# Kernel optimization log

Hardware: AMD Instinct MI355X
Metric: run time of the kernel (lower is better)

## Reference

```python
import jax, jax.numpy as jnp
import numpy as np

B, S, C, H, D = 2, 2048, 1024, 16, 64  # hidden C must equal H*D (value is a reshape of key_states)


def setup_inputs() -> dict:
    key = jax.random.key(0)
    ks = jax.random.split(key, 7)
    query_states = jax.random.normal(ks[0], (B, S, C), dtype=jnp.float32)
    key_states = jax.random.normal(ks[1], (B, S, C), dtype=jnp.float32)
    attention_mask = jax.random.randint(ks[2], (B, 1, 1, S), 0, 2).astype(jnp.int32)
    Wq = jax.random.normal(ks[3], (C, H, D), dtype=jnp.float32) * 0.02
    bq = jnp.zeros((H, D), dtype=jnp.float32)
    Wk = jax.random.normal(ks[4], (C, H, D), dtype=jnp.float32) * 0.02
    bk = jnp.zeros((H, D), dtype=jnp.float32)
    return {
        "query_states": query_states,
        "key_states": key_states,
        "attention_mask": attention_mask,
        "Wq": Wq,
        "bq": bq,
        "Wk": Wk,
        "bk": bk,
    }


def reference(query_states, key_states, attention_mask, Wq, bq, Wk, bk):
    # EinsumDense 'abc,cde->abde' with bias on 'de'
    q = jnp.einsum("bsc,chd->bshd", query_states, Wq) + bq  # [B,S,H,D]
    k = jnp.einsum("bsc,chd->bshd", key_states, Wk) + bk    # [B,S,H,D]
    # value is just key_states reshaped into head layout (no projection!)
    v = key_states.reshape(k.shape)                          # [B,S,H,D]
    # scale query by 1/sqrt(dk)
    q = q * jax.lax.rsqrt(jnp.asarray(D, q.dtype))
    # 'aecd,abcd->acbe': a=batch, c=head, b=query pos, e=key pos
    scores = jnp.einsum("bkhd,bqhd->bhqk", k, q)             # [B,H,Sq,Sk]
    mask = (1.0 - attention_mask.astype(scores.dtype)) * -10000.0
    scores = scores + mask
    probs = jax.nn.softmax(scores, axis=-1)
    # dropout is identity at training=False (default)
    # 'acbe,aecd->abcd': weighted sum of values over key positions
    out = jnp.einsum("bhqk,bkhd->bqhd", probs, v)            # [B,S,H,D]
    return out
```

## Files before the change

### kernel.cpp

```cpp
#include <hip/hip_runtime.h>

#define BSZ 2
#define SEQ 2048
#define CH  1024
#define NH  16
#define HD  64
#define LOG2E 1.4426950408889634f
#define MASKC (-14426.950408889634f)

typedef short  bf16x8 __attribute__((ext_vector_type(8)));
typedef short  bf16x4 __attribute__((ext_vector_type(4)));
typedef float  f32x4  __attribute__((ext_vector_type(4)));

__device__ __forceinline__ short f2bf(float f) {
    union { float f; unsigned u; } v; v.f = f;
    unsigned r = v.u + 0x7FFFu + ((v.u >> 16) & 1u);
    return (short)(r >> 16);
}
__device__ __forceinline__ short f2bf_fast(float f) {
    union { float f; unsigned u; } v; v.f = f;
    return (short)((v.u + 0x8000u) >> 16);
}
__device__ __forceinline__ float exp2_hw(float x) {
#if __has_builtin(__builtin_amdgcn_exp2f)
    return __builtin_amdgcn_exp2f(x);
#else
    float r;
    asm volatile("v_exp_f32 %0, %1\n\ts_nop 1" : "=v"(r) : "v"(x));
    return r;
#endif
}

#if __has_builtin(__builtin_amdgcn_mfma_f32_16x16x16bf16_1k)
__device__ __forceinline__ f32x4 mfma16x16x16(bf16x4 a, bf16x4 b, f32x4 c) {
    return __builtin_amdgcn_mfma_f32_16x16x16bf16_1k(a, b, c, 0, 0, 0);
}
#else
__device__ __forceinline__ f32x4 mfma16x16x16(bf16x4 a, bf16x4 b, f32x4 c) {
    f32x4 d;
    asm("v_mfma_f32_16x16x16_bf16 %0, %1, %2, %3"
        : "=v"(d) : "v"(a), "v"(b), "v"(c));
    return d;
}
#endif

__global__ __launch_bounds__(256) void prep(
    const float* __restrict__ query, const float* __restrict__ key,
    const float* __restrict__ Wq, const float* __restrict__ Wk,
    short* __restrict__ qc, short* __restrict__ kc,
    short* __restrict__ wtq, short* __restrict__ wtk,
    short* __restrict__ vtr)
{
    __shared__ float tile[64][65];
    const int bid = blockIdx.x;
    const int tid = threadIdx.x;

    if (bid < 4096) {
        const float* s = (bid < 2048) ? query : key;
        short*       d = (bid < 2048) ? qc : kc;
        long i = ((long)(bid & 2047) * 256 + tid) * 8;
        float4 v0 = *(const float4*)&s[i];
        float4 v1 = *(const float4*)&s[i + 4];
        bf16x8 o;
        o[0] = f2bf(v0.x); o[1] = f2bf(v0.y); o[2] = f2bf(v0.z); o[3] = f2bf(v0.w);
        o[4] = f2bf(v1.x); o[5] = f2bf(v1.y); o[6] = f2bf(v1.z); o[7] = f2bf(v1.w);
        *(bf16x8*)&d[i] = o;
        return;
    }

    const float* s; short* d;
    int r0, c0, srs, drs;
    if (bid < 4608) {
        int t = bid - 4096;
        s   = (t < 256) ? Wq : Wk;
        d   = (t < 256) ? wtq : wtk;
        t  &= 255;
        r0  = (t >> 4) * 64;
        c0  = (t & 15) * 64;
        srs = CH; drs = CH;
    } else {
        int t = bid - 4608;
        int z = t >> 5;
        int sy = t & 31;
        s   = key + (long)(z >> 4) * SEQ * CH + (long)(z & 15) * HD;
        d   = vtr + (long)z * HD * SEQ;
        r0  = sy * 64;
        c0  = 0;
        srs = CH; drs = SEQ;
    }

    const int r  = tid >> 2;
    const int c4 = (tid & 3) << 4;
    #pragma unroll
    for (int i = 0; i < 16; i += 4) {
        float4 v = *(const float4*)&s[(long)(r0 + r) * srs + c0 + c4 + i];
        tile[r][c4 + i + 0] = v.x;
        tile[r][c4 + i + 1] = v.y;
        tile[r][c4 + i + 2] = v.z;
        tile[r][c4 + i + 3] = v.w;
    }
    __syncthreads();
    bf16x8 o0, o1;
    #pragma unroll
    for (int i = 0; i < 8; i++) o0[i] = f2bf(tile[c4 + i][r]);
    #pragma unroll
    for (int i = 0; i < 8; i++) o1[i] = f2bf(tile[c4 + 8 + i][r]);
    *(bf16x8*)&d[(long)(c0 + r) * drs + r0 + c4 + 0] = o0;
    *(bf16x8*)&d[(long)(c0 + r) * drs + r0 + c4 + 8] = o1;
}

__global__ __launch_bounds__(256, 2) void proj_mfma(
    const short* __restrict__ Xq, const short* __restrict__ Xk,
    const short* __restrict__ Wtq, const short* __restrict__ Wtk,
    const float* __restrict__ bq_, const float* __restrict__ bk_,
    short* __restrict__ Yq, short* __restrict__ Yk)
{
    __shared__ short At[2][128 * 72];
    __shared__ short Bt[2][128 * 72];

    const int bid  = blockIdx.x;
    const int g    = bid >> 3, xcd = bid & 7;
    const int pair = ((g >> 3) << 3) | xcd;
    const int xt   = g & 7;
    const int yy   = pair >> 1;
    const int zz   = pair & 1;

    const short* X    = zz ? Xk  : Xq;
    const short* Wt   = zz ? Wtk : Wtq;
    const float* bias = zz ? bk_ : bq_;
    short*       Y    = zz ? Yk  : Yq;
    const float scale = zz ? 1.0f : (0.125f * LOG2E);

    const int tid  = threadIdx.x;
    const int lane = tid & 63, w = tid >> 6;
    const int quad = lane >> 4, t16 = lane & 15;
    const int m0 = yy * 128, n0 = xt * 128;
    const int srow = tid >> 1;
    const int shalf = (tid & 1) * 32;

    f32x4 acc[4][4];
    #pragma unroll
    for (int i = 0; i < 4; i++)
        #pragma unroll
        for (int j = 0; j < 4; j++)
            acc[i][j] = (f32x4){0.f, 0.f, 0.f, 0.f};

    const int M0 = (w >> 1) * 64, N0 = (w & 1) * 64;
    const int NIT = CH / 64;

    bf16x8 ar[4], br[4];
    #pragma unroll
    for (int c = 0; c < 4; c++) {
        ar[c] = *(const bf16x8*)&X [(long)(m0 + srow) * CH + shalf + 8 * c];
        br[c] = *(const bf16x8*)&Wt[(long)(n0 + srow) * CH + shalf + 8 * c];
    }
    #pragma unroll
    for (int c = 0; c < 4; c++) {
        *(bf16x8*)&At[0][srow * 72 + shalf + 8 * c] = ar[c];
        *(bf16x8*)&Bt[0][srow * 72 + shalf + 8 * c] = br[c];
    }
    #pragma unroll
    for (int c = 0; c < 4; c++) {
        ar[c] = *(const bf16x8*)&X [(long)(m0 + srow) * CH + 64 + shalf + 8 * c];
        br[c] = *(const bf16x8*)&Wt[(long)(n0 + srow) * CH + 64 + shalf + 8 * c];
    }
    __syncthreads();

    for (int it = 0; it < NIT; it++) {
        const int buf = it & 1;
        if (it + 1 < NIT) {
            #pragma unroll
            for (int c = 0; c < 4; c++) {
                *(bf16x8*)&At[buf ^ 1][srow * 72 + shalf + 8 * c] = ar[c];
                *(bf16x8*)&Bt[buf ^ 1][srow * 72 + shalf + 8 * c] = br[c];
            }
            if (it + 2 < NIT) {
                const long ko = (long)(it + 2) * 64;
                #pragma unroll
                for (int c = 0; c < 4; c++) {
                    ar[c] = *(const bf16x8*)&X [(long)(m0 + srow) * CH + ko + shalf + 8 * c];
                    br[c] = *(const bf16x8*)&Wt[(long)(n0 + srow) * CH + ko + shalf + 8 * c];
                }
            }
        }

        #pragma unroll
        for (int kk = 0; kk < 2; kk++) {
            bf16x8 af[4], bw[4];
            #pragma unroll
            for (int im = 0; im < 4; im++)
                af[im] = *(bf16x8*)&At[buf][(M0 + 16 * im + t16) * 72 + kk * 32 + quad * 8];
            #pragma unroll
            for (int jn = 0; jn < 4; jn++)
                bw[jn] = *(bf16x8*)&Bt[buf][(N0 + 16 * jn + t16) * 72 + kk * 32 + quad * 8];
            #pragma unroll
            for (int im = 0; im < 4; im++)
                #pragma unroll
                for (int jn = 0; jn < 4; jn++)
                    acc[im][jn] = __builtin_amdgcn_mfma_f32_16x16x32_bf16(
                        af[im], bw[jn], acc[im][jn], 0, 0, 0);
        }
        __syncthreads();
    }

    #pragma unroll
    for (int jn = 0; jn < 4; jn++) {
        float bs = bias[n0 + N0 + 16 * jn + t16];
        #pragma unroll
        for (int im = 0; im < 4; im++)
            #pragma unroll
            for (int reg = 0; reg < 4; reg++) {
                float y = (acc[im][jn][reg] + bs) * scale;
                Y[(long)(m0 + M0 + 16 * im + 4 * quad + reg) * (NH * HD)
                  + n0 + N0 + 16 * jn + t16] = f2bf(y);
            }
    }
}

__global__ __launch_bounds__(256, 2) void attn_mfma(
    const short* __restrict__ qp,
    const short* __restrict__ kp,
    const short* __restrict__ vt,
    const int*   __restrict__ amask,
    float* __restrict__ out)
{
    __shared__ short Kt[2][128 * 72];
    __shared__ short Vt[2][64 * 136];
    __shared__ float Msk[SEQ];

    const int bid = blockIdx.x;
    const int g   = bid >> 3, xcd = bid & 7;
    const int hb  = ((g >> 4) << 3) | xcd;
    const int qt  = g & 15;

    const int qt0 = qt * 128;
    const int h   = hb & 15;
    const int b   = hb >> 4;
    const int tid = threadIdx.x;
    const int lane = tid & 63, w = tid >> 6;
    const int quad = lane >> 4, t16 = lane & 15;

    {
        int4 a0 = *(const int4*)&amask[b * SEQ + tid * 8];
        int4 a1 = *(const int4*)&amask[b * SEQ + tid * 8 + 4];
        float4 f0 = {a0.x ? 0.f : MASKC, a0.y ? 0.f : MASKC,
                     a0.z ? 0.f : MASKC, a0.w ? 0.f : MASKC};
        float4 f1 = {a1.x ? 0.f : MASKC, a1.y ? 0.f : MASKC,
                     a1.z ? 0.f : MASKC, a1.w ? 0.f : MASKC};
        *(float4*)&Msk[tid * 8]     = f0;
        *(float4*)&Msk[tid * 8 + 4] = f1;
    }

    bf16x8 qf[2][2];
    #pragma unroll
    for (int qm = 0; qm < 2; qm++)
        #pragma unroll
        for (int ds = 0; ds < 2; ds++)
            qf[qm][ds] = *(const bf16x8*)&qp[
                (long)(b * SEQ + qt0 + w * 32 + qm * 16 + t16) * CH
                + h * HD + ds * 32 + quad * 8];

    f32x4 oa[4][2];
    float l_r[2];
    #pragma unroll
    for (int dt = 0; dt < 4; dt++)
        #pragma unroll
        for (int qm = 0; qm < 2; qm++)
            oa[dt][qm] = (f32x4){0.f, 0.f, 0.f, 0.f};
    l_r[0] = l_r[1] = 0.f;

    const int ksrow = tid >> 1;
    const int kscol = (tid & 1) * 32;
    const int vsrow = tid >> 2;
    const int vscol = (tid & 3) * 32;
    const long kbase = (long)(b * SEQ) * CH + h * HD;
    const long vbase = ((long)(b * NH + h) * HD) * SEQ;
    const int NIT = SEQ / 128;

    bf16x8 kr[4], vr[4];
    #pragma unroll
    for (int c = 0; c < 4; c++) {
        kr[c] = *(const bf16x8*)&kp[kbase + (long)ksrow * CH + kscol + 8 * c];
        vr[c] = *(const bf16x8*)&vt[vbase + (long)vsrow * SEQ + vscol + 8 * c];
    }
    #pragma unroll
    for (int c = 0; c < 4; c++) {
        *(bf16x8*)&Kt[0][ksrow * 72 + kscol + 8 * c] = kr[c];
        *(bf16x8*)&Vt[0][vsrow * 136 + vscol + 8 * c] = vr[c];
    }
    #pragma unroll
    for (int c = 0; c < 4; c++) {
        kr[c] = *(const bf16x8*)&kp[kbase + (long)(128 + ksrow) * CH + kscol + 8 * c];
        vr[c] = *(const bf16x8*)&vt[vbase + (long)vsrow * SEQ + 128 + vscol + 8 * c];
    }
    __syncthreads();

    for (int it = 0; it < NIT; it++) {
        const int buf = it & 1;
        const int kt0 = it * 128;

        if (it + 1 < NIT) {
            #pragma unroll
            for (int c = 0; c < 4; c++) {
                *(bf16x8*)&Kt[buf ^ 1][ksrow * 72 + kscol + 8 * c] = kr[c];
                *(bf16x8*)&Vt[buf ^ 1][vsrow * 136 + vscol + 8 * c] = vr[c];
            }
            if (it + 2 < NIT) {
                const int kn = kt0 + 256;
                #pragma unroll
                for (int c = 0; c < 4; c++) {
                    kr[c] = *(const bf16x8*)&kp[kbase + (long)(kn + ksrow) * CH + kscol + 8 * c];
                    vr[c] = *(const bf16x8*)&vt[vbase + (long)vsrow * SEQ + kn + vscol + 8 * c];
                }
            }
        }

        #pragma unroll
        for (int sub = 0; sub < 2; sub++) {
            const int ko = sub * 64;

            float4 mv4[4];
            #pragma unroll
            for (int jt = 0; jt < 4; jt++)
                mv4[jt] = *(const float4*)&Msk[kt0 + ko + jt * 16 + quad * 4];

            f32x4 sa[2][4];
            #pragma unroll
            for (int qm = 0; qm < 2; qm++)
                #pragma unroll
                for (int jt = 0; jt < 4; jt++)
                    sa[qm][jt] = (f32x4){mv4[jt].x, mv4[jt].y, mv4[jt].z, mv4[jt].w};
            #pragma unroll
            for (int ds = 0; ds < 2; ds++) {
                bf16x8 kb[4];
                #pragma unroll
                for (int jt = 0; jt < 4; jt++)
                    kb[jt] = *(bf16x8*)&Kt[buf][(ko + jt * 16 + t16) * 72 + ds * 32 + quad * 8];
                __builtin_amdgcn_s_setprio(1);
                #pragma unroll
                for (int qm = 0; qm < 2; qm++)
                    #pragma unroll
                    for (int jt = 0; jt < 4; jt++)
                        sa[qm][jt] = __builtin_amdgcn_mfma_f32_16x16x32_bf16(
                            kb[jt], qf[qm][ds], sa[qm][jt], 0, 0, 0);
                __builtin_amdgcn_s_setprio(0);
            }

            #pragma unroll
            for (int jt = 0; jt < 4; jt++) {
                bf16x4 pbq[2];
                #pragma unroll
                for (int qm = 0; qm < 2; qm++) {
                    float p0 = exp2_hw(sa[qm][jt][0]);
                    float p1 = exp2_hw(sa[qm][jt][1]);
                    float p2 = exp2_hw(sa[qm][jt][2]);
                    float p3 = exp2_hw(sa[qm][jt][3]);
                    l_r[qm] += (p0 + p1) + (p2 + p3);
                    bf16x4 pk;
                    pk[0] = f2bf_fast(p0); pk[1] = f2bf_fast(p1);
                    pk[2] = f2bf_fast(p2); pk[3] = f2bf_fast(p3);
                    pbq[qm] = pk;
                }
                bf16x4 va[4];
                #pragma unroll
                for (int dt = 0; dt < 4; dt++)
                    va[dt] = *(bf16x4*)&Vt[buf][(dt * 16 + t16) * 136 + ko + jt * 16 + quad * 4];
                __builtin_amdgcn_s_setprio(1);
                #pragma unroll
                for (int dt = 0; dt < 4; dt++)
                    #pragma unroll
                    for (int qm = 0; qm < 2; qm++)
                        oa[dt][qm] = mfma16x16x16(va[dt], pbq[qm], oa[dt][qm]);
                __builtin_amdgcn_s_setprio(0);
            }
        }
        __syncthreads();
    }

    #pragma unroll
    for (int qm = 0; qm < 2; qm++) {
        float l = l_r[qm];
        l += __shfl_xor(l, 16, 64);
        l += __shfl_xor(l, 32, 64);
        float inv = 1.0f / l;
        int q = qt0 + w * 32 + qm * 16 + t16;
        #pragma unroll
        for (int dt = 0; dt < 4; dt++) {
            f32x4 o = oa[dt][qm];
            float4 st = {o[0] * inv, o[1] * inv, o[2] * inv, o[3] * inv};
            *(float4*)&out[((long)(b * SEQ + q) * NH + h) * HD + dt * 16 + quad * 4] = st;
        }
    }
}

extern "C" void kernel_launch(void* const* d_in, const int* in_sizes, int n_in,
                              void* d_out, int out_size, void* d_ws, size_t ws_size,
                              hipStream_t stream) {
    const float* query = (const float*)d_in[0];
    const float* key   = (const float*)d_in[1];
    const int*   amask = (const int*)d_in[2];
    const float* Wq    = (const float*)d_in[3];
    const float* bq    = (const float*)d_in[4];
    const float* Wk    = (const float*)d_in[5];
    const float* bk    = (const float*)d_in[6];
    float* out = (float*)d_out;

    char* ws = (char*)d_ws;
    const long MB = 1024 * 1024;
    short* qc  = (short*)(ws + 0 * MB);
    short* kc  = (short*)(ws + 8 * MB);
    short* qp  = (short*)(ws + 16 * MB);
    short* kp  = (short*)(ws + 24 * MB);
    short* vtr = (short*)(ws + 32 * MB);
    short* wtq = (short*)(ws + 40 * MB);
    short* wtk = (short*)(ws + 42 * MB);

    prep<<<dim3(5632), 256, 0, stream>>>(query, key, Wq, Wk, qc, kc, wtq, wtk, vtr);

    proj_mfma<<<dim3(512), 256, 0, stream>>>(qc, kc, wtq, wtk, bq, bk, qp, kp);

    attn_mfma<<<dim3(512), 256, 0, stream>>>(qp, kp, vtr, amask, out);
}
```

Before: 172.2 us.

## Fuse fp32-to-bf16 activation conversion into projection GEMM loads

Removes the separate prep pass that converted query and key activations to bf16. The projection kernel now reads fp32 activations directly and converts them in registers while staging tiles, which drops one full write and re-read of two 8 MB buffers. Global load traffic inside the GEMM doubles for the A operand, and the extra conversion ALU work sits in the load path. It also replaces the manual softmax probability packing with the hardware packed bf16 convert instruction, which rounds to nearest-even.

```diff
diff --git a/kernel.cpp b/kernel.cpp
--- a/kernel.cpp
+++ b/kernel.cpp
@@ -17,9 +17,11 @@
     unsigned r = v.u + 0x7FFFu + ((v.u >> 16) & 1u);
     return (short)(r >> 16);
 }
-__device__ __forceinline__ short f2bf_fast(float f) {
-    union { float f; unsigned u; } v; v.f = f;
-    return (short)((v.u + 0x8000u) >> 16);
+__device__ __forceinline__ bf16x8 cvt8(float4 a, float4 b) {
+    bf16x8 o;
+    o[0] = f2bf(a.x); o[1] = f2bf(a.y); o[2] = f2bf(a.z); o[3] = f2bf(a.w);
+    o[4] = f2bf(b.x); o[5] = f2bf(b.y); o[6] = f2bf(b.z); o[7] = f2bf(b.w);
+    return o;
 }
 __device__ __forceinline__ float exp2_hw(float x) {
 #if __has_builtin(__builtin_amdgcn_exp2f)
@@ -31,6 +33,18 @@
 #endif
 }
 
+__device__ __forceinline__ bf16x4 pack4_rne(float p0, float p1, float p2, float p3) {
+    unsigned lo, hi;
+    asm("s_nop 1\n\t"
+        "v_cvt_pk_bf16_f32 %0, %2, %3\n\t"
+        "v_cvt_pk_bf16_f32 %1, %4, %5"
+        : "=&v"(lo), "=&v"(hi)
+        : "v"(p0), "v"(p1), "v"(p2), "v"(p3));
+    union { unsigned u[2]; bf16x4 v; } r;
+    r.u[0] = lo; r.u[1] = hi;
+    return r.v;
+}
+
 #if __has_builtin(__builtin_amdgcn_mfma_f32_16x16x16bf16_1k)
 __device__ __forceinline__ f32x4 mfma16x16x16(bf16x4 a, bf16x4 b, f32x4 c) {
     return __builtin_amdgcn_mfma_f32_16x16x16bf16_1k(a, b, c, 0, 0, 0);
@@ -45,9 +59,8 @@
 #endif
 
 __global__ __launch_bounds__(256) void prep(
-    const float* __restrict__ query, const float* __restrict__ key,
+    const float* __restrict__ key,
     const float* __restrict__ Wq, const float* __restrict__ Wk,
-    short* __restrict__ qc, short* __restrict__ kc,
     short* __restrict__ wtq, short* __restrict__ wtk,
     short* __restrict__ vtr)
 {
@@ -55,31 +68,17 @@
     const int bid = blockIdx.x;
     const int tid = threadIdx.x;
 
-    if (bid < 4096) {
-        const float* s = (bid < 2048) ? query : key;
-        short*       d = (bid < 2048) ? qc : kc;
-        long i = ((long)(bid & 2047) * 256 + tid) * 8;
-        float4 v0 = *(const float4*)&s[i];
-        float4 v1 = *(const float4*)&s[i + 4];
-        bf16x8 o;
-        o[0] = f2bf(v0.x); o[1] = f2bf(v0.y); o[2] = f2bf(v0.z); o[3] = f2bf(v0.w);
-        o[4] = f2bf(v1.x); o[5] = f2bf(v1.y); o[6] = f2bf(v1.z); o[7] = f2bf(v1.w);
-        *(bf16x8*)&d[i] = o;
-        return;
-    }
-
     const float* s; short* d;
     int r0, c0, srs, drs;
-    if (bid < 4608) {
-        int t = bid - 4096;
-        s   = (t < 256) ? Wq : Wk;
-        d   = (t < 256) ? wtq : wtk;
-        t  &= 255;
+    if (bid < 512) {
+        int t = bid & 255;
+        s   = (bid < 256) ? Wq : Wk;
+        d   = (bid < 256) ? wtq : wtk;
         r0  = (t >> 4) * 64;
         c0  = (t & 15) * 64;
         srs = CH; drs = CH;
     } else {
-        int t = bid - 4608;
+        int t = bid - 512;
         int z = t >> 5;
         int sy = t & 31;
         s   = key + (long)(z >> 4) * SEQ * CH + (long)(z & 15) * HD;
@@ -110,7 +109,7 @@
 }
 
 __global__ __launch_bounds__(256, 2) void proj_mfma(
-    const short* __restrict__ Xq, const short* __restrict__ Xk,
+    const float* __restrict__ Xq, const float* __restrict__ Xk,
     const short* __restrict__ Wtq, const short* __restrict__ Wtk,
     const float* __restrict__ bq_, const float* __restrict__ bk_,
     short* __restrict__ Yq, short* __restrict__ Yk)
@@ -125,7 +124,7 @@
     const int yy   = pair >> 1;
     const int zz   = pair & 1;
 
-    const short* X    = zz ? Xk  : Xq;
+    const float* X    = zz ? Xk  : Xq;
     const short* Wt   = zz ? Wtk : Wtq;
     const float* bias = zz ? bk_ : bq_;
     short*       Y    = zz ? Yk  : Yq;
@@ -151,7 +150,9 @@
     bf16x8 ar[4], br[4];
     #pragma unroll
     for (int c = 0; c < 4; c++) {
-        ar[c] = *(const bf16x8*)&X [(long)(m0 + srow) * CH + shalf + 8 * c];
+        float4 f0 = *(const float4*)&X[(long)(m0 + srow) * CH + shalf + 8 * c];
+        float4 f1 = *(const float4*)&X[(long)(m0 + srow) * CH + shalf + 8 * c + 4];
+        ar[c] = cvt8(f0, f1);
         br[c] = *(const bf16x8*)&Wt[(long)(n0 + srow) * CH + shalf + 8 * c];
     }
     #pragma unroll
@@ -161,7 +162,9 @@
     }
     #pragma unroll
     for (int c = 0; c < 4; c++) {
-        ar[c] = *(const bf16x8*)&X [(long)(m0 + srow) * CH + 64 + shalf + 8 * c];
+        float4 f0 = *(const float4*)&X[(long)(m0 + srow) * CH + 64 + shalf + 8 * c];
+        float4 f1 = *(const float4*)&X[(long)(m0 + srow) * CH + 64 + shalf + 8 * c + 4];
+        ar[c] = cvt8(f0, f1);
         br[c] = *(const bf16x8*)&Wt[(long)(n0 + srow) * CH + 64 + shalf + 8 * c];
     }
     __syncthreads();
@@ -178,7 +181,9 @@
                 const long ko = (long)(it + 2) * 64;
                 #pragma unroll
                 for (int c = 0; c < 4; c++) {
-                    ar[c] = *(const bf16x8*)&X [(long)(m0 + srow) * CH + ko + shalf + 8 * c];
+                    float4 f0 = *(const float4*)&X[(long)(m0 + srow) * CH + ko + shalf + 8 * c];
+                    float4 f1 = *(const float4*)&X[(long)(m0 + srow) * CH + ko + shalf + 8 * c + 4];
+                    ar[c] = cvt8(f0, f1);
                     br[c] = *(const bf16x8*)&Wt[(long)(n0 + srow) * CH + ko + shalf + 8 * c];
                 }
             }
@@ -356,10 +361,7 @@
                     float p2 = exp2_hw(sa[qm][jt][2]);
                     float p3 = exp2_hw(sa[qm][jt][3]);
                     l_r[qm] += (p0 + p1) + (p2 + p3);
-                    bf16x4 pk;
-                    pk[0] = f2bf_fast(p0); pk[1] = f2bf_fast(p1);
-                    pk[2] = f2bf_fast(p2); pk[3] = f2bf_fast(p3);
-                    pbq[qm] = pk;
+                    pbq[qm] = pack4_rne(p0, p1, p2, p3);
                 }
                 bf16x4 va[4];
                 #pragma unroll
@@ -407,17 +409,15 @@
 
     char* ws = (char*)d_ws;
     const long MB = 1024 * 1024;
-    short* qc  = (short*)(ws + 0 * MB);
-    short* kc  = (short*)(ws + 8 * MB);
-    short* qp  = (short*)(ws + 16 * MB);
-    short* kp  = (short*)(ws + 24 * MB);
-    short* vtr = (short*)(ws + 32 * MB);
-    short* wtq = (short*)(ws + 40 * MB);
-    short* wtk = (short*)(ws + 42 * MB);
-
-    prep<<<dim3(5632), 256, 0, stream>>>(query, key, Wq, Wk, qc, kc, wtq, wtk, vtr);
-
-    proj_mfma<<<dim3(512), 256, 0, stream>>>(qc, kc, wtq, wtk, bq, bk, qp, kp);
+    short* qp  = (short*)(ws + 0 * MB);
+    short* kp  = (short*)(ws + 8 * MB);
+    short* vtr = (short*)(ws + 16 * MB);
+    short* wtq = (short*)(ws + 24 * MB);
+    short* wtk = (short*)(ws + 26 * MB);
+
+    prep<<<dim3(1536), 256, 0, stream>>>(key, Wq, Wk, wtq, wtk, vtr);
+
+    proj_mfma<<<dim3(512), 256, 0, stream>>>(query, key, wtq, wtk, bq, bk, qp, kp);
 
     attn_mfma<<<dim3(512), 256, 0, stream>>>(qp, kp, vtr, amask, out);
 }
```

Result: slower. 190.9 us (+10.8%).
